# Performance work log

Measured on AMD Instinct MI355X. Metric: run time of the kernel, lower is better.

The kernel has to match this reference:

```python
import jax, jax.numpy as jnp
import numpy as np

N = 100000      # nodes
E = 3200000     # edges (avg degree 32)
DU = 256        # unary_channels
DP = 256        # pairwise_channels (== out_channels, required by fusion cat)
H = 64          # hidden_channels = out_channels // 4
DO = 256        # out_channels
STEPS = 1
EPS = 1e-5      # BatchNorm eps (torch default)


def _bn(h, gamma, beta):
    # BatchNorm1d, training-mode batch stats (biased variance, as torch normalizes)
    mu = jnp.mean(h, axis=0)
    var = jnp.var(h, axis=0)
    return gamma * (h - mu) * jax.lax.rsqrt(var + EPS) + beta


def setup_inputs() -> dict:
    key = jax.random.key(0)
    ks = jax.random.split(key, 12)
    edge_index = jax.random.randint(ks[0], (2, E), 0, N, dtype=jnp.int64)
    return {
        "x": jax.random.normal(ks[1], (N, DU), dtype=jnp.float32),
        "y": jax.random.normal(ks[2], (N, DP), dtype=jnp.float32),
        "pos": jax.random.normal(ks[3], (N, 3), dtype=jnp.float32),
        "edge_index": edge_index,
        "Wu": jax.random.normal(ks[4], (DU, H), dtype=jnp.float32) / np.sqrt(DU),
        "gu": jnp.ones((H,), jnp.float32), "bu": jnp.zeros((H,), jnp.float32),
        "Wp": jax.random.normal(ks[5], (DP, H), dtype=jnp.float32) / np.sqrt(DP),
        "gp": jnp.ones((H,), jnp.float32), "bp": jnp.zeros((H,), jnp.float32),
        "c": jnp.eye(H, dtype=jnp.float32) + 0.1 * jax.random.normal(ks[6], (H, H), dtype=jnp.float32),
        "Wm": jax.random.normal(ks[7], (H, DO), dtype=jnp.float32) / np.sqrt(H),
        "gm": jnp.ones((DO,), jnp.float32), "bm": jnp.zeros((DO,), jnp.float32),
        "Wf": jax.random.normal(ks[8], (2 * DO, DO), dtype=jnp.float32) / np.sqrt(2 * DO),
        "gf": jnp.ones((DO,), jnp.float32), "bf": jnp.zeros((DO,), jnp.float32),
    }


def reference(x, y, pos, edge_index, Wu, gu, bu, Wp, gp, bp, c, Wm, gm, bm, Wf, gf, bf):
    i, j = edge_index[0], edge_index[1]
    # unary / pairwise embeddings (Linear no-bias + BN)
    xu = _bn(x @ Wu, gu, bu)                      # [N, H]
    su = _bn(y @ Wp, gp, bp)                      # [N, H]
    # edge logits: -||s_i - s_j||^2, softmax grouped by destination i
    d = su[i] - su[j]                             # [E, H]
    logit = -jnp.sum(d * d, axis=1, keepdims=True)  # [E, 1]
    m = jax.ops.segment_max(logit, i, num_segments=N)
    ex = jnp.exp(logit - m[i])
    denom = jax.ops.segment_sum(ex, i, num_segments=N)
    s = ex / (denom[i] + 1e-16)                   # [E, 1] edge softmax weights
    # CRF mean-field iterations with linear solve
    z = xu
    C = c.T @ c                                   # [H, H]
    Minv = jnp.linalg.inv(jnp.eye(H, dtype=x.dtype) + C)
    h = xu
    for _ in range(STEPS):
        agg = jax.ops.segment_sum(s * h[j], i, num_segments=N)  # gather-scale-scatter
        h = (z + agg @ C) @ Minv
    # output heads
    h = jax.nn.leaky_relu(_bn(h @ Wm, gm, bm))
    out = jax.nn.leaky_relu(_bn(jnp.concatenate([h, y], axis=-1) @ Wf, gf, bf))
    return out
```

## Files before the change

kernel.cpp:

```cpp
#include <hip/hip_runtime.h>
#include <hip/hip_fp16.h>
#include <math.h>

typedef unsigned short u16;
typedef short s16x8 __attribute__((ext_vector_type(8)));
typedef unsigned short u16x8 __attribute__((ext_vector_type(8)));
typedef _Float16 f16x8 __attribute__((ext_vector_type(8)));
typedef float f32x4 __attribute__((ext_vector_type(4)));

__device__ __forceinline__ float bf2f(u16 u) {
  unsigned x = ((unsigned)u) << 16;
  return __uint_as_float(x);
}
__device__ __forceinline__ u16 f2bf(float f) {
  unsigned x = __float_as_uint(f);
  unsigned r = x + 0x7FFFu + ((x >> 16) & 1u);
  return (u16)(r >> 16);
}
__device__ __forceinline__ u16 f2h(float f) {
  __half h = __float2half_rn(f);
  return *reinterpret_cast<u16*>(&h);
}

static const size_t OFF_MINV   = 0;
static const size_t OFF_AU     = 32ull * 1024;
static const size_t OFF_BUE    = 32ull * 1024 + 256;
static const size_t OFF_AP     = 32ull * 1024 + 512;
static const size_t OFF_APBE   = 32ull * 1024 + 768;
static const size_t OFF_AM     = 36ull * 1024;
static const size_t OFF_BM     = 37ull * 1024;
static const size_t OFF_AF     = 38ull * 1024;
static const size_t OFF_BF     = 39ull * 1024;
static const size_t OFF_BTOT   = 40ull * 1024;
static const size_t OFF_BOFF   = 44ull * 1024;
static const size_t OFF_WUT    = 64ull * 1024;
static const size_t OFF_WMT    = 128ull * 1024;
static const size_t OFF_WFT    = 192ull * 1024;
static const size_t OFF_WPH    = 512ull * 1024;
static const size_t OFF_PART1A = 1ull  * 1024 * 1024;
static const size_t OFF_PART1B = 1ull  * 1024 * 1024 + 512 * 1024;
static const size_t OFF_PART2A = 2ull  * 1024 * 1024;
static const size_t OFF_PART2B = 2ull  * 1024 * 1024 + 512 * 1024;
static const size_t OFF_ROWPTR = 3ull  * 1024 * 1024;
static const size_t OFF_BLKCNT = 5ull  * 1024 * 1024;
static const size_t OFF_SRCJ   = 18ull * 1024 * 1024;
static const size_t OFF_U      = 44ull * 1024 * 1024;
static const size_t OFF_P      = 70ull * 1024 * 1024;
static const size_t OFF_PS     = 109ull * 1024 * 1024;
static const size_t OFF_H2     = 122ull * 1024 * 1024;

#define NBLK_BIN 1024

__global__ __launch_bounds__(256) void k_prep(const float* __restrict__ c,
                                              float* __restrict__ minv_out) {
  __shared__ float CC[4096];
  __shared__ float aug[64 * 129];
  __shared__ float fs[64];
  float* cl = aug;
  int t = threadIdx.x;
  for (int idx = t; idx < 4096; idx += 256) cl[idx] = c[idx];
  __syncthreads();
  for (int idx = t; idx < 4096; idx += 256) {
    int a = idx >> 6, b = idx & 63;
    float s = (a == b) ? 1.f : 0.f;
    for (int k = 0; k < 64; ++k) s += cl[k * 64 + a] * cl[k * 64 + b];
    CC[idx] = s;
  }
  __syncthreads();
  for (int idx = t; idx < 8192; idx += 256) {
    int r = idx >> 7, cc = idx & 127;
    aug[r * 129 + cc] = (cc < 64) ? CC[r * 64 + cc] : (((cc - 64) == r) ? 1.f : 0.f);
  }
  __syncthreads();
  int cloc = t & 127;
  int rbase = t >> 7;
  for (int p = 0; p < 64; ++p) {
    if (t < 64) fs[t] = (t == p) ? 0.f : aug[t * 129 + p] / aug[p * 129 + p];
    __syncthreads();
    float pc = aug[p * 129 + cloc];
#pragma unroll
    for (int rr = 0; rr < 64; rr += 2) {
      int r = rr + rbase;
      aug[r * 129 + cloc] -= fs[r] * pc;
    }
    __syncthreads();
  }
  for (int idx = t; idx < 4096; idx += 256) {
    int r = idx >> 6, cc = idx & 63;
    minv_out[idx] = aug[r * 129 + 64 + cc] / aug[r * 129 + r];
  }
}

__global__ __launch_bounds__(256) void k_tcvt_all(const float* __restrict__ Wu, const float* __restrict__ Wm,
                                                  const float* __restrict__ Wf, const float* __restrict__ Wp,
                                                  u16* __restrict__ WUT, u16* __restrict__ WMT,
                                                  u16* __restrict__ WFT, u16* __restrict__ WPH) {
  int b = blockIdx.x, t = threadIdx.x;
  if (b < 64) {
    int i = b * 256 + t;
    int k = i >> 6, n = i & 63;
    WUT[(size_t)n * 256 + k] = f2bf(Wu[i]);
  } else if (b < 128) {
    int i = (b - 64) * 256 + t;
    int k = i >> 8, n = i & 255;
    WMT[(size_t)n * 64 + k] = f2bf(Wm[i]);
  } else if (b < 640) {
    int i = (b - 128) * 256 + t;
    int k = i >> 8, n = i & 255;
    WFT[(size_t)n * 512 + k] = f2bf(Wf[i]);
  } else {
    int i = (b - 640) * 256 + t;
    int k = i >> 6, n = i & 63;
    WPH[(size_t)n * 256 + k] = f2h(Wp[i]);
  }
}

__global__ __launch_bounds__(256) void kA1(const int* __restrict__ ei, int E, int chunk,
                                           int* __restrict__ blockCnt, int nbk) {
  __shared__ int c[512];
  int t = threadIdx.x, bid = blockIdx.x;
  c[t] = 0; c[t + 256] = 0;
  __syncthreads();
  int e0 = bid * chunk, e1 = min(E, e0 + chunk);
  for (int e = e0 + t; e < e1; e += 256) atomicAdd(&c[ei[e] >> 8], 1);
  __syncthreads();
  for (int b = t; b < nbk; b += 256) blockCnt[(size_t)bid * nbk + b] = c[b];
}

__global__ __launch_bounds__(256) void kA2(int* __restrict__ blockCnt, int nbk,
                                           int* __restrict__ bucketTot) {
  int b = blockIdx.x, t = threadIdx.x;
  int base = t * 4;
  int v0 = blockCnt[(size_t)(base + 0) * nbk + b];
  int v1 = blockCnt[(size_t)(base + 1) * nbk + b];
  int v2 = blockCnt[(size_t)(base + 2) * nbk + b];
  int v3 = blockCnt[(size_t)(base + 3) * nbk + b];
  int s1 = v0 + v1, s2 = s1 + v2, tot = s2 + v3;
  __shared__ int ps[256];
  ps[t] = tot;
  __syncthreads();
  for (int off = 1; off < 256; off <<= 1) {
    int a = (t >= off) ? ps[t - off] : 0;
    __syncthreads();
    ps[t] += a;
    __syncthreads();
  }
  int ex = (t > 0) ? ps[t - 1] : 0;
  blockCnt[(size_t)(base + 0) * nbk + b] = ex;
  blockCnt[(size_t)(base + 1) * nbk + b] = ex + v0;
  blockCnt[(size_t)(base + 2) * nbk + b] = ex + s1;
  blockCnt[(size_t)(base + 3) * nbk + b] = ex + s2;
  if (t == 255) bucketTot[b] = ps[255];
}

__global__ __launch_bounds__(512) void kA2b(const int* __restrict__ bucketTot,
                                            int* __restrict__ bucketOff, int nbk) {
  __shared__ int s[512];
  int t = threadIdx.x;
  s[t] = (t < nbk) ? bucketTot[t] : 0;
  __syncthreads();
  for (int off = 1; off < 512; off <<= 1) {
    int a = (t >= off) ? s[t - off] : 0;
    __syncthreads();
    s[t] += a;
    __syncthreads();
  }
  if (t == 0) bucketOff[0] = 0;
  if (t < nbk) bucketOff[t + 1] = s[t];
}

__global__ __launch_bounds__(256) void kA3(const int* __restrict__ ei, const int* __restrict__ ej,
                                           int E, int chunk,
                                           const int* __restrict__ blockExc,
                                           const int* __restrict__ bucketOff,
                                           int nbk, unsigned* __restrict__ tmp) {
  __shared__ int c[512], off[512], gb[512], cur[512];
  __shared__ uint2 stage[4096];
  int t = threadIdx.x, bid = blockIdx.x;
  c[t] = 0; c[t + 256] = 0;
  __syncthreads();
  int e0 = bid * chunk, e1 = min(E, e0 + chunk);
  int m = e1 - e0;
  for (int e = e0 + t; e < e1; e += 256) atomicAdd(&c[ei[e] >> 8], 1);
  __syncthreads();
  int v0 = c[t], v1 = c[t + 256];
  off[t] = v0; off[t + 256] = v1;
  __syncthreads();
  for (int o = 1; o < 512; o <<= 1) {
    int a0 = (t >= o) ? off[t - o] : 0;
    int a1 = ((t + 256) >= o) ? off[t + 256 - o] : 0;
    __syncthreads();
    off[t] += a0; off[t + 256] += a1;
    __syncthreads();
  }
  int ex0 = off[t] - v0, ex1 = off[t + 256] - v1;
  if (t < nbk)
    gb[t] = bucketOff[t] + blockExc[(size_t)bid * nbk + t] - ex0;
  if (t + 256 < nbk)
    gb[t + 256] = bucketOff[t + 256] + blockExc[(size_t)bid * nbk + t + 256] - ex1;
  cur[t] = ex0; cur[t + 256] = ex1;
  __syncthreads();
  for (int e = e0 + t; e < e1; e += 256) {
    int i = ei[e];
    int p = atomicAdd(&cur[i >> 8], 1);
    stage[p] = make_uint2((unsigned)i, (unsigned)ej[e]);
  }
  __syncthreads();
  for (int s = t; s < m; s += 256) {
    uint2 v = stage[s];
    tmp[gb[v.x >> 8] + s] = ((v.x & 255u) << 24) | v.y;
  }
}

#define BCAP 12288
__global__ __launch_bounds__(256) void kB(const unsigned* __restrict__ tmp,
                                          const int* __restrict__ bucketOff,
                                          int nbk, int N, int E,
                                          int* __restrict__ rowptr, int* __restrict__ srcj) {
  __shared__ int cnt[256], sc[256], cur[256];
  __shared__ int jbuf[BCAP];
  int b = blockIdx.x, t = threadIdx.x;
  int nb0 = b << 8;
  int e0 = bucketOff[b], e1 = bucketOff[b + 1];
  int m = e1 - e0;
  cnt[t] = 0;
  __syncthreads();
  for (int s = t; s < m; s += 256) atomicAdd(&cnt[tmp[e0 + s] >> 24], 1);
  __syncthreads();
  int v = cnt[t];
  sc[t] = v;
  __syncthreads();
  for (int off = 1; off < 256; off <<= 1) {
    int a = (t >= off) ? sc[t - off] : 0;
    __syncthreads();
// ... 110 lines not shown
          if constexpr (FP16) {
            f16x8 af = *(const f16x8*)pa;
            f16x8 bf = *(const f16x8*)pb;
            acc[m][n] = __builtin_amdgcn_mfma_f32_16x16x32_f16(af, bf, acc[m][n], 0, 0, 0);
          } else {
            s16x8 af = *(const s16x8*)pa;
            s16x8 bf = *(const s16x8*)pb;
            acc[m][n] = __builtin_amdgcn_mfma_f32_16x16x32_bf16(af, bf, acc[m][n], 0, 0, 0);
          }
        }
      }
    }
  };

  loadTile(0);
  dswrite(0);
  __syncthreads();
  for (int kk = 0; kk < nK; ++kk) {
    int b = kk & 1;
    if (kk + 1 < nK) loadTile(kk + 1);
    compute(b);
    if (kk + 1 < nK) { dswrite(b ^ 1); __syncthreads(); }
  }

#pragma unroll
  for (int m = 0; m < 4; ++m) {
#pragma unroll
    for (int n = 0; n < FN; ++n) {
      int col = n0 + wc * WN + n * 16 + lr;
#pragma unroll
      for (int q = 0; q < 4; ++q) {
        int row = m0 + wr * 64 + m * 16 + lk * 4 + q;
        if (row < M) {
          if constexpr (OBF) Cb[(size_t)row * ldC + col] = f2bf(acc[m][n][q]);
          else               Cf[(size_t)row * ldC + col] = acc[m][n][q];
        }
      }
    }
  }

  if constexpr (STATS) {
    __syncthreads();
    float* sb = (float*)&lds[0][0];
#pragma unroll
    for (int n = 0; n < FN; ++n) {
      float s1 = 0.f, s2 = 0.f;
#pragma unroll
      for (int m = 0; m < 4; ++m)
#pragma unroll
        for (int q = 0; q < 4; ++q) {
          int row = m0 + wr * 64 + m * 16 + lk * 4 + q;
          float v = (row < M) ? acc[m][n][q] : 0.f;
          s1 += v; s2 += v * v;
        }
      s1 += __shfl_xor(s1, 16); s2 += __shfl_xor(s2, 16);
      s1 += __shfl_xor(s1, 32); s2 += __shfl_xor(s2, 32);
      if (lk == 0) {
        int c = wc * WN + n * 16 + lr;
        sb[(wr * BN + c) * 2 + 0] = s1;
        sb[(wr * BN + c) * 2 + 1] = s2;
      }
    }
    __syncthreads();
    if (t < BN) {
      float s1 = sb[t * 2]     + sb[(BN + t) * 2];
      float s2 = sb[t * 2 + 1] + sb[(BN + t) * 2 + 1];
      p1[(size_t)blockIdx.x * ncTot + n0 + t] = s1;
      p2[(size_t)blockIdx.x * ncTot + n0 + t] = s2;
// ... 200 lines not shown
    }
  }
}

__global__ __launch_bounds__(256) void k_reduce_fin(const float* __restrict__ part1,
                                                    const float* __restrict__ part2,
                                                    int nb, int C, float invN,
                                                    const float* __restrict__ gamma,
                                                    const float* __restrict__ beta,
                                                    float* __restrict__ a_out,
                                                    float* __restrict__ b_out) {
  int c = blockIdx.x;
  int t = threadIdx.x;
  float s1 = 0.f, s2 = 0.f;
  for (int b = t; b < nb; b += 256) {
    s1 += part1[(size_t)b * C + c];
    s2 += part2[(size_t)b * C + c];
  }
  for (int m = 32; m; m >>= 1) { s1 += __shfl_xor(s1, m); s2 += __shfl_xor(s2, m); }
  __shared__ float l1[4], l2[4];
  if ((t & 63) == 0) { l1[t >> 6] = s1; l2[t >> 6] = s2; }
  __syncthreads();
  if (t == 0) {
    s1 = l1[0] + l1[1] + l1[2] + l1[3];
    s2 = l2[0] + l2[1] + l2[2] + l2[3];
    float mu  = s1 * invN;
    float var = s2 * invN - mu * mu;
    float a = gamma[c] * rsqrtf(var + 1e-5f);
    a_out[c] = a;
    b_out[c] = beta[c] - mu * a;
  }
}

__global__ __launch_bounds__(256) void k_scaleP(const float* __restrict__ P, const float* __restrict__ ap,
                                                __half* __restrict__ PS, int n8) {
  for (int i = blockIdx.x * 256 + threadIdx.x; i < n8; i += gridDim.x * 256) {
    int c0 = (i & 7) * 8;
    float4 s0 = *(const float4*)(ap + c0), s1 = *(const float4*)(ap + c0 + 4);
    float4 a = ((const float4*)P)[i * 2];
    float4 b = ((const float4*)P)[i * 2 + 1];
    __half2 o0 = __floats2half2_rn(a.x * s0.x, a.y * s0.y);
    __half2 o1 = __floats2half2_rn(a.z * s0.z, a.w * s0.w);
    __half2 o2 = __floats2half2_rn(b.x * s1.x, b.y * s1.y);
    __half2 o3 = __floats2half2_rn(b.z * s1.z, b.w * s1.w);
    uint4 out;
    out.x = *(unsigned*)&o0; out.y = *(unsigned*)&o1;
    out.z = *(unsigned*)&o2; out.w = *(unsigned*)&o3;
    ((uint4*)PS)[i] = out;
  }
}

__global__ __launch_bounds__(256) void k_nodeall(const __half* __restrict__ PS,
                                                 const int* __restrict__ srcj,
                                                 const int* __restrict__ rowptr,
                                                 const u16* __restrict__ UB,
                                                 const float* __restrict__ au,
                                                 const float* __restrict__ bue,
                                                 const float* __restrict__ minv,
                                                 int N, u16* __restrict__ HB) {
  __shared__ float mS[4096];
  __shared__ float zma[4][64];
  int t = threadIdx.x;
  for (int idx = t; idx < 1024; idx += 256)
    ((float4*)mS)[idx] = ((const float4*)minv)[idx];
  __syncthreads();

  int lane = t & 63, wid = t >> 6;
  int node = blockIdx.x * 4 + wid;
  if (node >= N) return;

  int lane8 = lane & 7, g8 = lane >> 3;
  const uint4* P4 = (const uint4*)PS;
  uint4 uv = P4[(size_t)node * 8 + lane8];
  float2 u0 = __half22float2(*(const __half2*)&uv.x);
  float2 u1 = __half22float2(((const __half2*)&uv.x)[1]);
  float2 u2 = __half22float2(*(const __half2*)&uv.z);
  float2 u3 = __half22float2(((const __half2*)&uv.z)[1]);
  float psl = __half2float(PS[(size_t)node * 64 + lane]);
  int b0 = rowptr[node], b1 = rowptr[node + 1];
  int deg = b1 - b0;
  float aggv = 0.f;
  if (deg > 0) {
    int cnt = deg < 64 ? deg : 64;
    int jj = (lane < cnt) ? srcj[b0 + lane] : 0;
    float lg = -INFINITY;
    int capbase = lane & ~7;
    int capsrc  = (lane & 7) << 3;
    for (int ss = 0; ss < cnt; ss += 8) {
      int sl = ss + g8; if (sl >= cnt) sl = cnt - 1;
      int j = __shfl(jj, sl);
      uint4 vv = P4[(size_t)j * 8 + lane8];
      float2 v0 = __half22float2(*(const __half2*)&vv.x);
      float2 v1 = __half22float2(((const __half2*)&vv.x)[1]);
      float2 v2 = __half22float2(*(const __half2*)&vv.z);
      float2 v3 = __half22float2(((const __half2*)&vv.z)[1]);
      float d0 = u0.x - v0.x, d1 = u0.y - v0.y;
      float d2 = u1.x - v1.x, d3 = u1.y - v1.y;
      float d4 = u2.x - v2.x, d5 = u2.y - v2.y;
      float d6 = u3.x - v3.x, d7 = u3.y - v3.y;
      float p = d0*d0 + d1*d1 + d2*d2 + d3*d3 + d4*d4 + d5*d5 + d6*d6 + d7*d7;
      p += __shfl_xor(p, 1, 8);
      p += __shfl_xor(p, 2, 8);
      p += __shfl_xor(p, 4, 8);
      float val = __shfl(p, capsrc);
      if (ss == capbase && lane < cnt) lg = -val;
    }
    float mx = lg;
    for (int s = b0 + 64; s < b1; ++s) {
      int j = srcj[s];
      float d = psl - __half2float(PS[(size_t)j * 64 + lane]);
      float p = d * d;
      for (int m = 32; m; m >>= 1) p += __shfl_xor(p, m);
      mx = fmaxf(mx, -p);
    }
    for (int m = 32; m; m >>= 1) mx = fmaxf(mx, __shfl_xor(mx, m));
    float ex = (lane < cnt) ? __expf(lg - mx) : 0.f;
    float sm = ex;
    for (int s = b0 + 64; s < b1; ++s) {
      int j = srcj[s];
      float d = psl - __half2float(PS[(size_t)j * 64 + lane]);
      float p = d * d;
      for (int m = 32; m; m >>= 1) p += __shfl_xor(p, m);
      if (lane == 0) sm += __expf(-p - mx);
    }
    for (int m = 32; m; m >>= 1) sm += __shfl_xor(sm, m);
    float inv = 1.0f / (sm + 1e-16f);
    float w = ex * inv;
    float acc = 0.f;
    int ss = 0;
    for (; ss + 8 <= cnt; ss += 8) {
      int   j0 = __shfl(jj, ss),     j1 = __shfl(jj, ss + 1);
      int   j2 = __shfl(jj, ss + 2), j3 = __shfl(jj, ss + 3);
      int   j4 = __shfl(jj, ss + 4), j5 = __shfl(jj, ss + 5);
      int   j6 = __shfl(jj, ss + 6), j7 = __shfl(jj, ss + 7);
      float w0 = __shfl(w, ss),      w1 = __shfl(w, ss + 1);
      float w2 = __shfl(w, ss + 2),  w3 = __shfl(w, ss + 3);
      float w4 = __shfl(w, ss + 4),  w5 = __shfl(w, ss + 5);
      float w6 = __shfl(w, ss + 6),  w7 = __shfl(w, ss + 7);
      float v0 = bf2f(UB[(size_t)j0 * 64 + lane]);
      float v1 = bf2f(UB[(size_t)j1 * 64 + lane]);
      float v2 = bf2f(UB[(size_t)j2 * 64 + lane]);
      float v3 = bf2f(UB[(size_t)j3 * 64 + lane]);
      float v4 = bf2f(UB[(size_t)j4 * 64 + lane]);
      float v5 = bf2f(UB[(size_t)j5 * 64 + lane]);
      float v6 = bf2f(UB[(size_t)j6 * 64 + lane]);
      float v7 = bf2f(UB[(size_t)j7 * 64 + lane]);
      acc += w0 * v0 + w1 * v1 + w2 * v2 + w3 * v3;
      acc += w4 * v4 + w5 * v5 + w6 * v6 + w7 * v7;
    }
    for (; ss < cnt; ++ss) {
      int j0 = __shfl(jj, ss);
      float w0 = __shfl(w, ss);
      acc += w0 * bf2f(UB[(size_t)j0 * 64 + lane]);
    }
    for (int s = b0 + 64; s < b1; ++s) {
      int j = srcj[s];
      float d = psl - __half2float(PS[(size_t)j * 64 + lane]);
      float p = d * d;
      for (int m = 32; m; m >>= 1) p += __shfl_xor(p, m);
      acc += __expf(-p - mx) * inv * bf2f(UB[(size_t)j * 64 + lane]);
    }
    aggv = au[lane] * acc + bue[lane];
  }
  float z = au[lane] * bf2f(UB[(size_t)node * 64 + lane]) + bue[lane];
  zma[wid][lane] = z - aggv;
  float h = aggv;
#pragma unroll 8
  for (int k = 0; k < 64; ++k) h += zma[wid][k] * mS[k * 64 + lane];
  HB[(size_t)node * 64 + lane] = f2bf(h);
}

__global__ __launch_bounds__(256) void k_bnact16(const u16* __restrict__ raw, const float* __restrict__ af,
                                                 const float* __restrict__ bfp, float* __restrict__ out, int n8) {
  int i = blockIdx.x * 256 + threadIdx.x;
  int stride = gridDim.x * 256;
  for (; i < n8; i += stride) {
    int c0 = (i & 31) * 8;
    float av[8], bv[8];
    *(float4*)(av) = *(const float4*)(af + c0);  *(float4*)(av + 4) = *(const float4*)(af + c0 + 4);
    *(float4*)(bv) = *(const float4*)(bfp + c0); *(float4*)(bv + 4) = *(const float4*)(bfp + c0 + 4);
    u16x8 r = ((const u16x8*)raw)[i];
    float o[8];
#pragma unroll
    for (int j = 0; j < 8; ++j) {
      float v = bf2f((u16)r[j]) * av[j] + bv[j];
      o[j] = (v > 0.f) ? v : 0.01f * v;
    }
    ((float4*)out)[i * 2]     = *(float4*)(o);
    ((float4*)out)[i * 2 + 1] = *(float4*)(o + 4);
  }
// ... 16 lines not shown
  const float* gm   = (const float*)d_in[12];
  const float* bm   = (const float*)d_in[13];
  const float* Wf   = (const float*)d_in[14];
  const float* gf   = (const float*)d_in[15];
  const float* bfv  = (const float*)d_in[16];

  const int N = in_sizes[0] / 256;
  const int E = in_sizes[3] / 2;
  const int* ei = eidx;
  const int* ej = eidx + E;

  char* ws = (char*)d_ws;
  float* MINV  = (float*)(ws + OFF_MINV);
  float* AU    = (float*)(ws + OFF_AU);
  float* BUE   = (float*)(ws + OFF_BUE);
  float* AP    = (float*)(ws + OFF_AP);
  float* APBE  = (float*)(ws + OFF_APBE);
  float* AM    = (float*)(ws + OFF_AM);
  float* BM    = (float*)(ws + OFF_BM);
  float* AF    = (float*)(ws + OFF_AF);
  float* BF    = (float*)(ws + OFF_BF);
  int*   BTOT  = (int*)(ws + OFF_BTOT);
  int*   BOFF  = (int*)(ws + OFF_BOFF);
  u16*   WUT   = (u16*)(ws + OFF_WUT);
  u16*   WMT   = (u16*)(ws + OFF_WMT);
  u16*   WFT   = (u16*)(ws + OFF_WFT);
  u16*   WPH   = (u16*)(ws + OFF_WPH);
  float* PART1A= (float*)(ws + OFF_PART1A);
  float* PART1B= (float*)(ws + OFF_PART1B);
  float* PART2A= (float*)(ws + OFF_PART2A);
  float* PART2B= (float*)(ws + OFF_PART2B);
  int*   ROWPTR= (int*)(ws + OFF_ROWPTR);
  int*   BLKCNT= (int*)(ws + OFF_BLKCNT);
  u16*   HB    = (u16*)(ws + OFF_BLKCNT);
  int*   SRCJ  = (int*)(ws + OFF_SRCJ);
  u16*   RAWO  = (u16*)(ws + OFF_SRCJ);
  u16*   UBRAW = (u16*)(ws + OFF_U);
  unsigned* TMP= (unsigned*)(ws + OFF_P);
  float* P     = (float*)(ws + OFF_P);
  __half* PS   = (__half*)(ws + OFF_PS);
  u16*   H2    = (u16*)(ws + OFF_H2);

  const float invN = 1.0f / (float)N;
  const int mtiles   = (N + 127) / 128;
  const int n8_64    = N * 64 / 8;
  const int n8_256   = N * 256 / 8;
  const int nbk      = (N + 255) >> 8;
  const int chunk    = (E + NBLK_BIN - 1) / NBLK_BIN;

  k_prep<<<1, 256, 0, stream>>>(cIn, MINV);
  k_tcvt_all<<<704, 256, 0, stream>>>(Wu, Wm, Wf, Wp, WUT, WMT, WFT, WPH);

  kA1<<<NBLK_BIN, 256, 0, stream>>>(ei, E, chunk, BLKCNT, nbk);
  kA2<<<nbk, 256, 0, stream>>>(BLKCNT, nbk, BTOT);
  kA2b<<<1, 512, 0, stream>>>(BTOT, BOFF, nbk);
  kA3<<<NBLK_BIN, 256, 0, stream>>>(ei, ej, E, chunk, BLKCNT, BOFF, nbk, TMP);
  kB<<<nbk, 256, 0, stream>>>(TMP, BOFF, nbk, N, E, ROWPTR, SRCJ);

  k_mfma<64, 2, 1, 1, 0><<<dim3(mtiles, 1), 256, 0, stream>>>(
      nullptr, x, 256, 256, N, WUT, nullptr, UBRAW, 64, 64, PART1A, PART2A);

  k_mfma<64, 2, 0, 1, 1><<<dim3(mtiles, 1), 256, 0, stream>>>(
      nullptr, y, 256, 256, N, WPH, P, nullptr, 64, 64, PART1B, PART2B);

  k_reduce2<<<128, 256, 0, stream>>>(PART1A, PART2A, PART1B, PART2B, mtiles, invN,
                                     gu, bu, gp, bp, AU, BUE, AP, APBE);
  k_scaleP<<<1024, 256, 0, stream>>>(P, AP, PS, n8_64);

  k_nodeall<<<(N + 3) / 4, 256, 0, stream>>>(PS, SRCJ, ROWPTR, UBRAW, AU, BUE, MINV, N, HB);

  k_mfma2<0><<<mtiles, 512, 0, stream>>>(
      HB, 64, 64, N, nullptr, nullptr, nullptr, nullptr, WMT, H2, PART1A, PART2A);
  k_reduce_fin<<<256, 256, 0, stream>>>(PART1A, PART2A, mtiles, 256, invN, gm, bm, AM, BM);

  k_mfma2<1><<<mtiles, 512, 0, stream>>>(
      nullptr, 0, 512, N, H2, y, AM, BM, WFT, RAWO, PART1A, PART2A);
  k_reduce_fin<<<256, 256, 0, stream>>>(PART1A, PART2A, mtiles, 256, invN, gf, bfv, AF, BF);
  k_bnact16<<<2048, 256, 0, stream>>>(RAWO, AF, BF, (float*)d_out, n8_256);
}
```

Before: 527.3 us.

## Fold BN scale into node kernel, fuse prep kernels, reuse bin counts, unroll gathers

The pairwise GEMM now writes fp16 output directly, and the BN scale is applied inside the node kernel, so the separate fp32 P buffer and k_scaleP pass are gone. The matrix-inverse prep is merged into the weight-conversion launch as an extra block. The binning pass reuses per-block counts from kA1 instead of recounting edges in kA3, storing offsets in a new buffer. The node kernel also processes 16 neighbours per iteration in both the logit and aggregation loops to expose more memory parallelism. Storing unscaled fp16 values may change rounding, and the larger unroll raises register pressure.

```diff
diff --git a/kernel.cpp b/kernel.cpp
--- a/kernel.cpp
+++ b/kernel.cpp
@@ -43,6 +43,7 @@
 static const size_t OFF_PART2B = 2ull  * 1024 * 1024 + 512 * 1024;
 static const size_t OFF_ROWPTR = 3ull  * 1024 * 1024;
 static const size_t OFF_BLKCNT = 5ull  * 1024 * 1024;
+static const size_t OFF_BLKOFF = 7ull  * 1024 * 1024;
 static const size_t OFF_SRCJ   = 18ull * 1024 * 1024;
 static const size_t OFF_U      = 44ull * 1024 * 1024;
 static const size_t OFF_P      = 70ull * 1024 * 1024;
@@ -51,67 +52,67 @@
 
 #define NBLK_BIN 1024
 
-__global__ __launch_bounds__(256) void k_prep(const float* __restrict__ c,
-                                              float* __restrict__ minv_out) {
-  __shared__ float CC[4096];
-  __shared__ float aug[64 * 129];
-  __shared__ float fs[64];
-  float* cl = aug;
-  int t = threadIdx.x;
-  for (int idx = t; idx < 4096; idx += 256) cl[idx] = c[idx];
-  __syncthreads();
-  for (int idx = t; idx < 4096; idx += 256) {
-    int a = idx >> 6, b = idx & 63;
-    float s = (a == b) ? 1.f : 0.f;
-    for (int k = 0; k < 64; ++k) s += cl[k * 64 + a] * cl[k * 64 + b];
-    CC[idx] = s;
-  }
-  __syncthreads();
-  for (int idx = t; idx < 8192; idx += 256) {
-    int r = idx >> 7, cc = idx & 127;
-    aug[r * 129 + cc] = (cc < 64) ? CC[r * 64 + cc] : (((cc - 64) == r) ? 1.f : 0.f);
-  }
-  __syncthreads();
-  int cloc = t & 127;
-  int rbase = t >> 7;
-  for (int p = 0; p < 64; ++p) {
-    if (t < 64) fs[t] = (t == p) ? 0.f : aug[t * 129 + p] / aug[p * 129 + p];
-    __syncthreads();
-    float pc = aug[p * 129 + cloc];
-#pragma unroll
-    for (int rr = 0; rr < 64; rr += 2) {
-      int r = rr + rbase;
-      aug[r * 129 + cloc] -= fs[r] * pc;
-    }
-    __syncthreads();
-  }
-  for (int idx = t; idx < 4096; idx += 256) {
-    int r = idx >> 6, cc = idx & 63;
-    minv_out[idx] = aug[r * 129 + 64 + cc] / aug[r * 129 + r];
-  }
-}
-
-__global__ __launch_bounds__(256) void k_tcvt_all(const float* __restrict__ Wu, const float* __restrict__ Wm,
-                                                  const float* __restrict__ Wf, const float* __restrict__ Wp,
-                                                  u16* __restrict__ WUT, u16* __restrict__ WMT,
-                                                  u16* __restrict__ WFT, u16* __restrict__ WPH) {
+__global__ __launch_bounds__(256) void k_tcvt_prep(const float* __restrict__ Wu, const float* __restrict__ Wm,
+                                                   const float* __restrict__ Wf, const float* __restrict__ Wp,
+                                                   u16* __restrict__ WUT, u16* __restrict__ WMT,
+                                                   u16* __restrict__ WFT, u16* __restrict__ WPH,
+                                                   const float* __restrict__ c, float* __restrict__ minv_out) {
   int b = blockIdx.x, t = threadIdx.x;
   if (b < 64) {
     int i = b * 256 + t;
     int k = i >> 6, n = i & 63;
     WUT[(size_t)n * 256 + k] = f2bf(Wu[i]);
+    return;
   } else if (b < 128) {
     int i = (b - 64) * 256 + t;
     int k = i >> 8, n = i & 255;
     WMT[(size_t)n * 64 + k] = f2bf(Wm[i]);
+    return;
   } else if (b < 640) {
     int i = (b - 128) * 256 + t;
     int k = i >> 8, n = i & 255;
     WFT[(size_t)n * 512 + k] = f2bf(Wf[i]);
-  } else {
+    return;
+  } else if (b < 704) {
     int i = (b - 640) * 256 + t;
     int k = i >> 6, n = i & 63;
     WPH[(size_t)n * 256 + k] = f2h(Wp[i]);
+    return;
+  }
+  __shared__ float CC[4096];
+  __shared__ float aug[64 * 129];
+  __shared__ float fs[64];
+  float* cl = aug;
+  for (int idx = t; idx < 4096; idx += 256) cl[idx] = c[idx];
+  __syncthreads();
+  for (int idx = t; idx < 4096; idx += 256) {
+    int a = idx >> 6, bb = idx & 63;
+    float s = (a == bb) ? 1.f : 0.f;
+    for (int k = 0; k < 64; ++k) s += cl[k * 64 + a] * cl[k * 64 + bb];
+    CC[idx] = s;
+  }
+  __syncthreads();
+  for (int idx = t; idx < 8192; idx += 256) {
+    int r = idx >> 7, cc = idx & 127;
+    aug[r * 129 + cc] = (cc < 64) ? CC[r * 64 + cc] : (((cc - 64) == r) ? 1.f : 0.f);
+  }
+  __syncthreads();
+  int cloc = t & 127;
+  int rbase = t >> 7;
+  for (int p = 0; p < 64; ++p) {
+    if (t < 64) fs[t] = (t == p) ? 0.f : aug[t * 129 + p] / aug[p * 129 + p];
+    __syncthreads();
+    float pc = aug[p * 129 + cloc];
+#pragma unroll
+    for (int rr = 0; rr < 64; rr += 2) {
+      int r = rr + rbase;
+      aug[r * 129 + cloc] -= fs[r] * pc;
+    }
+    __syncthreads();
+  }
+  for (int idx = t; idx < 4096; idx += 256) {
+    int r = idx >> 6, cc = idx & 63;
+    minv_out[idx] = aug[r * 129 + 64 + cc] / aug[r * 129 + r];
   }
 }
 
@@ -127,8 +128,8 @@
   for (int b = t; b < nbk; b += 256) blockCnt[(size_t)bid * nbk + b] = c[b];
 }
 
-__global__ __launch_bounds__(256) void kA2(int* __restrict__ blockCnt, int nbk,
-                                           int* __restrict__ bucketTot) {
+__global__ __launch_bounds__(256) void kA2(const int* __restrict__ blockCnt, int nbk,
+                                           int* __restrict__ blkOff, int* __restrict__ bucketTot) {
   int b = blockIdx.x, t = threadIdx.x;
   int base = t * 4;
   int v0 = blockCnt[(size_t)(base + 0) * nbk + b];
@@ -146,10 +147,10 @@
     __syncthreads();
   }
   int ex = (t > 0) ? ps[t - 1] : 0;
-  blockCnt[(size_t)(base + 0) * nbk + b] = ex;
-  blockCnt[(size_t)(base + 1) * nbk + b] = ex + v0;
-  blockCnt[(size_t)(base + 2) * nbk + b] = ex + s1;
-  blockCnt[(size_t)(base + 3) * nbk + b] = ex + s2;
+  blkOff[(size_t)(base + 0) * nbk + b] = ex;
+  blkOff[(size_t)(base + 1) * nbk + b] = ex + v0;
+  blkOff[(size_t)(base + 2) * nbk + b] = ex + s1;
+  blkOff[(size_t)(base + 3) * nbk + b] = ex + s2;
   if (t == 255) bucketTot[b] = ps[255];
 }
 
@@ -171,19 +172,15 @@
 
 __global__ __launch_bounds__(256) void kA3(const int* __restrict__ ei, const int* __restrict__ ej,
                                            int E, int chunk,
-                                           const int* __restrict__ blockExc,
+                                           const int* __restrict__ blockCnt,
+                                           const int* __restrict__ blkOff,
                                            const int* __restrict__ bucketOff,
                                            int nbk, unsigned* __restrict__ tmp) {
-  __shared__ int c[512], off[512], gb[512], cur[512];
+  __shared__ int off[512], gb[512], cur[512];
   __shared__ uint2 stage[4096];
   int t = threadIdx.x, bid = blockIdx.x;
-  c[t] = 0; c[t + 256] = 0;
-  __syncthreads();
-  int e0 = bid * chunk, e1 = min(E, e0 + chunk);
-  int m = e1 - e0;
-  for (int e = e0 + t; e < e1; e += 256) atomicAdd(&c[ei[e] >> 8], 1);
-  __syncthreads();
-  int v0 = c[t], v1 = c[t + 256];
+  int v0 = (t < nbk) ? blockCnt[(size_t)bid * nbk + t] : 0;
+  int v1 = (t + 256 < nbk) ? blockCnt[(size_t)bid * nbk + t + 256] : 0;
   off[t] = v0; off[t + 256] = v1;
   __syncthreads();
   for (int o = 1; o < 512; o <<= 1) {
@@ -195,11 +192,13 @@
   }
   int ex0 = off[t] - v0, ex1 = off[t + 256] - v1;
   if (t < nbk)
-    gb[t] = bucketOff[t] + blockExc[(size_t)bid * nbk + t] - ex0;
+    gb[t] = bucketOff[t] + blkOff[(size_t)bid * nbk + t] - ex0;
   if (t + 256 < nbk)
-    gb[t + 256] = bucketOff[t + 256] + blockExc[(size_t)bid * nbk + t + 256] - ex1;
+    gb[t + 256] = bucketOff[t + 256] + blkOff[(size_t)bid * nbk + t + 256] - ex1;
   cur[t] = ex0; cur[t + 256] = ex1;
   __syncthreads();
+  int e0 = bid * chunk, e1 = min(E, e0 + chunk);
+  int m = e1 - e0;
   for (int e = e0 + t; e < e1; e += 256) {
     int i = ei[e];
     int p = atomicAdd(&cur[i >> 8], 1);
@@ -376,8 +375,9 @@
       for (int q = 0; q < 4; ++q) {
         int row = m0 + wr * 64 + m * 16 + lk * 4 + q;
         if (row < M) {
-          if constexpr (OBF) Cb[(size_t)row * ldC + col] = f2bf(acc[m][n][q]);
-          else               Cf[(size_t)row * ldC + col] = acc[m][n][q];
+          if constexpr (OBF == 2)      Cb[(size_t)row * ldC + col] = f2h(acc[m][n][q]);
+          else if constexpr (OBF == 1) Cb[(size_t)row * ldC + col] = f2bf(acc[m][n][q]);
+          else                         Cf[(size_t)row * ldC + col] = acc[m][n][q];
         }
       }
     }
@@ -644,30 +644,13 @@
   }
 }
 
-__global__ __launch_bounds__(256) void k_scaleP(const float* __restrict__ P, const float* __restrict__ ap,
-                                                __half* __restrict__ PS, int n8) {
-  for (int i = blockIdx.x * 256 + threadIdx.x; i < n8; i += gridDim.x * 256) {
-    int c0 = (i & 7) * 8;
-    float4 s0 = *(const float4*)(ap + c0), s1 = *(const float4*)(ap + c0 + 4);
-    float4 a = ((const float4*)P)[i * 2];
-    float4 b = ((const float4*)P)[i * 2 + 1];
-    __half2 o0 = __floats2half2_rn(a.x * s0.x, a.y * s0.y);
-    __half2 o1 = __floats2half2_rn(a.z * s0.z, a.w * s0.w);
-    __half2 o2 = __floats2half2_rn(b.x * s1.x, b.y * s1.y);
-    __half2 o3 = __floats2half2_rn(b.z * s1.z, b.w * s1.w);
-    uint4 out;
-    out.x = *(unsigned*)&o0; out.y = *(unsigned*)&o1;
-    out.z = *(unsigned*)&o2; out.w = *(unsigned*)&o3;
-    ((uint4*)PS)[i] = out;
-  }
-}
-
 __global__ __launch_bounds__(256) void k_nodeall(const __half* __restrict__ PS,
                                                  const int* __restrict__ srcj,
                                                  const int* __restrict__ rowptr,
                                                  const u16* __restrict__ UB,
                                                  const float* __restrict__ au,
                                                  const float* __restrict__ bue,
+                                                 const float* __restrict__ ap,
                                                  const float* __restrict__ minv,
                                                  int N, u16* __restrict__ HB) {
   __shared__ float mS[4096];
@@ -683,11 +666,17 @@
 
   int lane8 = lane & 7, g8 = lane >> 3;
   const uint4* P4 = (const uint4*)PS;
+  float av[8];
+  *(float4*)(av)     = *(const float4*)(ap + lane8 * 8);
+  *(float4*)(av + 4) = *(const float4*)(ap + lane8 * 8 + 4);
+  float apl = ap[lane];
   uint4 uv = P4[(size_t)node * 8 + lane8];
   float2 u0 = __half22float2(*(const __half2*)&uv.x);
   float2 u1 = __half22float2(((const __half2*)&uv.x)[1]);
   float2 u2 = __half22float2(*(const __half2*)&uv.z);
   float2 u3 = __half22float2(((const __half2*)&uv.z)[1]);
+  u0.x *= av[0]; u0.y *= av[1]; u1.x *= av[2]; u1.y *= av[3];
+  u2.x *= av[4]; u2.y *= av[5]; u3.x *= av[6]; u3.y *= av[7];
   float psl = __half2float(PS[(size_t)node * 64 + lane]);
   int b0 = rowptr[node], b1 = rowptr[node + 1];
   int deg = b1 - b0;
@@ -698,29 +687,53 @@
     float lg = -INFINITY;
     int capbase = lane & ~7;
     int capsrc  = (lane & 7) << 3;
-    for (int ss = 0; ss < cnt; ss += 8) {
-      int sl = ss + g8; if (sl >= cnt) sl = cnt - 1;
-      int j = __shfl(jj, sl);
-      uint4 vv = P4[(size_t)j * 8 + lane8];
+
+    auto logit8 = [&](uint4 vv) -> float {
       float2 v0 = __half22float2(*(const __half2*)&vv.x);
       float2 v1 = __half22float2(((const __half2*)&vv.x)[1]);
       float2 v2 = __half22float2(*(const __half2*)&vv.z);
       float2 v3 = __half22float2(((const __half2*)&vv.z)[1]);
-      float d0 = u0.x - v0.x, d1 = u0.y - v0.y;
-      float d2 = u1.x - v1.x, d3 = u1.y - v1.y;
-      float d4 = u2.x - v2.x, d5 = u2.y - v2.y;
-      float d6 = u3.x - v3.x, d7 = u3.y - v3.y;
-      float p = d0*d0 + d1*d1 + d2*d2 + d3*d3 + d4*d4 + d5*d5 + d6*d6 + d7*d7;
-      p += __shfl_xor(p, 1, 8);
-      p += __shfl_xor(p, 2, 8);
-      p += __shfl_xor(p, 4, 8);
-      float val = __shfl(p, capsrc);
-      if (ss == capbase && lane < cnt) lg = -val;
+      float d0 = fmaf(-av[0], v0.x, u0.x), d1 = fmaf(-av[1], v0.y, u0.y);
+      float d2 = fmaf(-av[2], v1.x, u1.x), d3 = fmaf(-av[3], v1.y, u1.y);
+      float d4 = fmaf(-av[4], v2.x, u2.x), d5 = fmaf(-av[5], v2.y, u2.y);
+      float d6 = fmaf(-av[6], v3.x, u3.x), d7 = fmaf(-av[7], v3.y, u3.y);
+      return d0*d0 + d1*d1 + d2*d2 + d3*d3 + d4*d4 + d5*d5 + d6*d6 + d7*d7;
+    };
+
+    int ss = 0;
+    while (ss < cnt) {
+      if (ss + 16 <= cnt) {
+        int jA = __shfl(jj, ss + g8);
+        int jB = __shfl(jj, ss + 8 + g8);
+        uint4 vvA = P4[(size_t)jA * 8 + lane8];
+        uint4 vvB = P4[(size_t)jB * 8 + lane8];
+        float pA = logit8(vvA);
+        float pB = logit8(vvB);
+        pA += __shfl_xor(pA, 1, 8); pB += __shfl_xor(pB, 1, 8);
+        pA += __shfl_xor(pA, 2, 8); pB += __shfl_xor(pB, 2, 8);
+        pA += __shfl_xor(pA, 4, 8); pB += __shfl_xor(pB, 4, 8);
+        float valA = __shfl(pA, capsrc);
+        float valB = __shfl(pB, capsrc);
+        if (ss == capbase && lane < cnt) lg = -valA;
+        if (ss + 8 == capbase && lane < cnt) lg = -valB;
+        ss += 16;
+      } else {
+        int sl = ss + g8; if (sl >= cnt) sl = cnt - 1;
+        int j = __shfl(jj, sl);
+        uint4 vv = P4[(size_t)j * 8 + lane8];
+        float p = logit8(vv);
+        p += __shfl_xor(p, 1, 8);
+        p += __shfl_xor(p, 2, 8);
+        p += __shfl_xor(p, 4, 8);
+        float val = __shfl(p, capsrc);
+        if (ss == capbase && lane < cnt) lg = -val;
+        ss += 8;
+      }
     }
     float mx = lg;
     for (int s = b0 + 64; s < b1; ++s) {
       int j = srcj[s];
-      float d = psl - __half2float(PS[(size_t)j * 64 + lane]);
+      float d = apl * (psl - __half2float(PS[(size_t)j * 64 + lane]));
       float p = d * d;
       for (int m = 32; m; m >>= 1) p += __shfl_xor(p, m);
       mx = fmaxf(mx, -p);
@@ -730,7 +743,7 @@
     float sm = ex;
     for (int s = b0 + 64; s < b1; ++s) {
       int j = srcj[s];
-      float d = psl - __half2float(PS[(size_t)j * 64 + lane]);
+      float d = apl * (psl - __half2float(PS[(size_t)j * 64 + lane]));
       float p = d * d;
       for (int m = 32; m; m >>= 1) p += __shfl_xor(p, m);
       if (lane == 0) sm += __expf(-p - mx);
@@ -739,26 +752,26 @@
     float inv = 1.0f / (sm + 1e-16f);
     float w = ex * inv;
     float acc = 0.f;
-    int ss = 0;
+    ss = 0;
+    for (; ss + 16 <= cnt; ss += 16) {
+      int jv[16]; float wv[16];
+#pragma unroll
+      for (int q = 0; q < 16; ++q) { jv[q] = __shfl(jj, ss + q); wv[q] = __shfl(w, ss + q); }
+      float vv[16];
+#pragma unroll
+      for (int q = 0; q < 16; ++q) vv[q] = bf2f(UB[(size_t)jv[q] * 64 + lane]);
+#pragma unroll
+      for (int q = 0; q < 16; ++q) acc += wv[q] * vv[q];
+    }
     for (; ss + 8 <= cnt; ss += 8) {
-      int   j0 = __shfl(jj, ss),     j1 = __shfl(jj, ss + 1);
-      int   j2 = __shfl(jj, ss + 2), j3 = __shfl(jj, ss + 3);
-      int   j4 = __shfl(jj, ss + 4), j5 = __shfl(jj, ss + 5);
-      int   j6 = __shfl(jj, ss + 6), j7 = __shfl(jj, ss + 7);
-      float w0 = __shfl(w, ss),      w1 = __shfl(w, ss + 1);
-      float w2 = __shfl(w, ss + 2),  w3 = __shfl(w, ss + 3);
-      float w4 = __shfl(w, ss + 4),  w5 = __shfl(w, ss + 5);
-      float w6 = __shfl(w, ss + 6),  w7 = __shfl(w, ss + 7);
-      float v0 = bf2f(UB[(size_t)j0 * 64 + lane]);
-      float v1 = bf2f(UB[(size_t)j1 * 64 + lane]);
-      float v2 = bf2f(UB[(size_t)j2 * 64 + lane]);
-      float v3 = bf2f(UB[(size_t)j3 * 64 + lane]);
-      float v4 = bf2f(UB[(size_t)j4 * 64 + lane]);
-      float v5 = bf2f(UB[(size_t)j5 * 64 + lane]);
-      float v6 = bf2f(UB[(size_t)j6 * 64 + lane]);
-      float v7 = bf2f(UB[(size_t)j7 * 64 + lane]);
-      acc += w0 * v0 + w1 * v1 + w2 * v2 + w3 * v3;
-      acc += w4 * v4 + w5 * v5 + w6 * v6 + w7 * v7;
+      int jv[8]; float wv[8];
+#pragma unroll
+      for (int q = 0; q < 8; ++q) { jv[q] = __shfl(jj, ss + q); wv[q] = __shfl(w, ss + q); }
+      float vv[8];
+#pragma unroll
+      for (int q = 0; q < 8; ++q) vv[q] = bf2f(UB[(size_t)jv[q] * 64 + lane]);
+#pragma unroll
+      for (int q = 0; q < 8; ++q) acc += wv[q] * vv[q];
     }
     for (; ss < cnt; ++ss) {
       int j0 = __shfl(jj, ss);
@@ -767,7 +780,7 @@
     }
     for (int s = b0 + 64; s < b1; ++s) {
       int j = srcj[s];
-      float d = psl - __half2float(PS[(size_t)j * 64 + lane]);
+      float d = apl * (psl - __half2float(PS[(size_t)j * 64 + lane]));
       float p = d * d;
       for (int m = 32; m; m >>= 1) p += __shfl_xor(p, m);
       acc += __expf(-p - mx) * inv * bf2f(UB[(size_t)j * 64 + lane]);
@@ -850,42 +863,39 @@
   float* PART2B= (float*)(ws + OFF_PART2B);
   int*   ROWPTR= (int*)(ws + OFF_ROWPTR);
   int*   BLKCNT= (int*)(ws + OFF_BLKCNT);
+  int*   BLKOFF= (int*)(ws + OFF_BLKOFF);
   u16*   HB    = (u16*)(ws + OFF_BLKCNT);
   int*   SRCJ  = (int*)(ws + OFF_SRCJ);
   u16*   RAWO  = (u16*)(ws + OFF_SRCJ);
   u16*   UBRAW = (u16*)(ws + OFF_U);
   unsigned* TMP= (unsigned*)(ws + OFF_P);
-  float* P     = (float*)(ws + OFF_P);
   __half* PS   = (__half*)(ws + OFF_PS);
   u16*   H2    = (u16*)(ws + OFF_H2);
 
   const float invN = 1.0f / (float)N;
   const int mtiles   = (N + 127) / 128;
-  const int n8_64    = N * 64 / 8;
   const int n8_256   = N * 256 / 8;
   const int nbk      = (N + 255) >> 8;
   const int chunk    = (E + NBLK_BIN - 1) / NBLK_BIN;
 
-  k_prep<<<1, 256, 0, stream>>>(cIn, MINV);
-  k_tcvt_all<<<704, 256, 0, stream>>>(Wu, Wm, Wf, Wp, WUT, WMT, WFT, WPH);
+  k_tcvt_prep<<<705, 256, 0, stream>>>(Wu, Wm, Wf, Wp, WUT, WMT, WFT, WPH, cIn, MINV);
 
   kA1<<<NBLK_BIN, 256, 0, stream>>>(ei, E, chunk, BLKCNT, nbk);
-  kA2<<<nbk, 256, 0, stream>>>(BLKCNT, nbk, BTOT);
+  kA2<<<nbk, 256, 0, stream>>>(BLKCNT, nbk, BLKOFF, BTOT);
   kA2b<<<1, 512, 0, stream>>>(BTOT, BOFF, nbk);
-  kA3<<<NBLK_BIN, 256, 0, stream>>>(ei, ej, E, chunk, BLKCNT, BOFF, nbk, TMP);
+  kA3<<<NBLK_BIN, 256, 0, stream>>>(ei, ej, E, chunk, BLKCNT, BLKOFF, BOFF, nbk, TMP);
   kB<<<nbk, 256, 0, stream>>>(TMP, BOFF, nbk, N, E, ROWPTR, SRCJ);
 
   k_mfma<64, 2, 1, 1, 0><<<dim3(mtiles, 1), 256, 0, stream>>>(
       nullptr, x, 256, 256, N, WUT, nullptr, UBRAW, 64, 64, PART1A, PART2A);
 
-  k_mfma<64, 2, 0, 1, 1><<<dim3(mtiles, 1), 256, 0, stream>>>(
-      nullptr, y, 256, 256, N, WPH, P, nullptr, 64, 64, PART1B, PART2B);
+  k_mfma<64, 2, 2, 1, 1><<<dim3(mtiles, 1), 256, 0, stream>>>(
+      nullptr, y, 256, 256, N, WPH, nullptr, (u16*)PS, 64, 64, PART1B, PART2B);
 
   k_reduce2<<<128, 256, 0, stream>>>(PART1A, PART2A, PART1B, PART2B, mtiles, invN,
                                      gu, bu, gp, bp, AU, BUE, AP, APBE);
-  k_scaleP<<<1024, 256, 0, stream>>>(P, AP, PS, n8_64);
-
-  k_nodeall<<<(N + 3) / 4, 256, 0, stream>>>(PS, SRCJ, ROWPTR, UBRAW, AU, BUE, MINV, N, HB);
+
+  k_nodeall<<<(N + 3) / 4, 256, 0, stream>>>(PS, SRCJ, ROWPTR, UBRAW, AU, BUE, AP, MINV, N, HB);
 
   k_mfma2<0><<<mtiles, 512, 0, stream>>>(
       HB, 64, 64, N, nullptr, nullptr, nullptr, nullptr, WMT, H2, PART1A, PART2A);
```

New measurement: 549.9 us. +4.3%, slower.

## Merge prep kernels, reuse bin counts in scatter, store pairwise GEMM as fp16

Applied to the files above, without the earlier changes.

The matrix-inverse prep is folded into the weight-conversion kernel as an extra block, which removes one launch. The binning scatter kernel now reads the per-block counts saved by the counting pass instead of recounting edges with shared atomics, so kA2 writes its offsets to a separate buffer. The pairwise GEMM now writes fp16 straight into PS, and the scale kernel rescales in place. That halves its traffic and drops the fp32 P buffer, with a small precision risk from rounding before the scale is applied.

```diff
diff --git a/kernel.cpp b/kernel.cpp
--- a/kernel.cpp
+++ b/kernel.cpp
@@ -43,6 +43,7 @@
 static const size_t OFF_PART2B = 2ull  * 1024 * 1024 + 512 * 1024;
 static const size_t OFF_ROWPTR = 3ull  * 1024 * 1024;
 static const size_t OFF_BLKCNT = 5ull  * 1024 * 1024;
+static const size_t OFF_BLKOFF = 7ull  * 1024 * 1024;
 static const size_t OFF_SRCJ   = 18ull * 1024 * 1024;
 static const size_t OFF_U      = 44ull * 1024 * 1024;
 static const size_t OFF_P      = 70ull * 1024 * 1024;
@@ -51,67 +52,67 @@
 
 #define NBLK_BIN 1024
 
-__global__ __launch_bounds__(256) void k_prep(const float* __restrict__ c,
-                                              float* __restrict__ minv_out) {
-  __shared__ float CC[4096];
-  __shared__ float aug[64 * 129];
-  __shared__ float fs[64];
-  float* cl = aug;
-  int t = threadIdx.x;
-  for (int idx = t; idx < 4096; idx += 256) cl[idx] = c[idx];
-  __syncthreads();
-  for (int idx = t; idx < 4096; idx += 256) {
-    int a = idx >> 6, b = idx & 63;
-    float s = (a == b) ? 1.f : 0.f;
-    for (int k = 0; k < 64; ++k) s += cl[k * 64 + a] * cl[k * 64 + b];
-    CC[idx] = s;
-  }
-  __syncthreads();
-  for (int idx = t; idx < 8192; idx += 256) {
-    int r = idx >> 7, cc = idx & 127;
-    aug[r * 129 + cc] = (cc < 64) ? CC[r * 64 + cc] : (((cc - 64) == r) ? 1.f : 0.f);
-  }
-  __syncthreads();
-  int cloc = t & 127;
-  int rbase = t >> 7;
-  for (int p = 0; p < 64; ++p) {
-    if (t < 64) fs[t] = (t == p) ? 0.f : aug[t * 129 + p] / aug[p * 129 + p];
-    __syncthreads();
-    float pc = aug[p * 129 + cloc];
-#pragma unroll
-    for (int rr = 0; rr < 64; rr += 2) {
-      int r = rr + rbase;
-      aug[r * 129 + cloc] -= fs[r] * pc;
-    }
-    __syncthreads();
-  }
-  for (int idx = t; idx < 4096; idx += 256) {
-    int r = idx >> 6, cc = idx & 63;
-    minv_out[idx] = aug[r * 129 + 64 + cc] / aug[r * 129 + r];
-  }
-}
-
-__global__ __launch_bounds__(256) void k_tcvt_all(const float* __restrict__ Wu, const float* __restrict__ Wm,
-                                                  const float* __restrict__ Wf, const float* __restrict__ Wp,
-                                                  u16* __restrict__ WUT, u16* __restrict__ WMT,
-                                                  u16* __restrict__ WFT, u16* __restrict__ WPH) {
+__global__ __launch_bounds__(256) void k_tcvt_prep(const float* __restrict__ Wu, const float* __restrict__ Wm,
+                                                   const float* __restrict__ Wf, const float* __restrict__ Wp,
+                                                   u16* __restrict__ WUT, u16* __restrict__ WMT,
+                                                   u16* __restrict__ WFT, u16* __restrict__ WPH,
+                                                   const float* __restrict__ c, float* __restrict__ minv_out) {
   int b = blockIdx.x, t = threadIdx.x;
   if (b < 64) {
     int i = b * 256 + t;
     int k = i >> 6, n = i & 63;
     WUT[(size_t)n * 256 + k] = f2bf(Wu[i]);
+    return;
   } else if (b < 128) {
     int i = (b - 64) * 256 + t;
     int k = i >> 8, n = i & 255;
     WMT[(size_t)n * 64 + k] = f2bf(Wm[i]);
+    return;
   } else if (b < 640) {
     int i = (b - 128) * 256 + t;
     int k = i >> 8, n = i & 255;
     WFT[(size_t)n * 512 + k] = f2bf(Wf[i]);
-  } else {
+    return;
+  } else if (b < 704) {
     int i = (b - 640) * 256 + t;
     int k = i >> 6, n = i & 63;
     WPH[(size_t)n * 256 + k] = f2h(Wp[i]);
+    return;
+  }
+  __shared__ float CC[4096];
+  __shared__ float aug[64 * 129];
+  __shared__ float fs[64];
+  float* cl = aug;
+  for (int idx = t; idx < 4096; idx += 256) cl[idx] = c[idx];
+  __syncthreads();
+  for (int idx = t; idx < 4096; idx += 256) {
+    int a = idx >> 6, bb = idx & 63;
+    float s = (a == bb) ? 1.f : 0.f;
+    for (int k = 0; k < 64; ++k) s += cl[k * 64 + a] * cl[k * 64 + bb];
+    CC[idx] = s;
+  }
+  __syncthreads();
+  for (int idx = t; idx < 8192; idx += 256) {
+    int r = idx >> 7, cc = idx & 127;
+    aug[r * 129 + cc] = (cc < 64) ? CC[r * 64 + cc] : (((cc - 64) == r) ? 1.f : 0.f);
+  }
+  __syncthreads();
+  int cloc = t & 127;
+  int rbase = t >> 7;
+  for (int p = 0; p < 64; ++p) {
+    if (t < 64) fs[t] = (t == p) ? 0.f : aug[t * 129 + p] / aug[p * 129 + p];
+    __syncthreads();
+    float pc = aug[p * 129 + cloc];
+#pragma unroll
+    for (int rr = 0; rr < 64; rr += 2) {
+      int r = rr + rbase;
+      aug[r * 129 + cloc] -= fs[r] * pc;
+    }
+    __syncthreads();
+  }
+  for (int idx = t; idx < 4096; idx += 256) {
+    int r = idx >> 6, cc = idx & 63;
+    minv_out[idx] = aug[r * 129 + 64 + cc] / aug[r * 129 + r];
   }
 }
 
@@ -127,8 +128,8 @@
   for (int b = t; b < nbk; b += 256) blockCnt[(size_t)bid * nbk + b] = c[b];
 }
 
-__global__ __launch_bounds__(256) void kA2(int* __restrict__ blockCnt, int nbk,
-                                           int* __restrict__ bucketTot) {
+__global__ __launch_bounds__(256) void kA2(const int* __restrict__ blockCnt, int nbk,
+                                           int* __restrict__ blkOff, int* __restrict__ bucketTot) {
   int b = blockIdx.x, t = threadIdx.x;
   int base = t * 4;
   int v0 = blockCnt[(size_t)(base + 0) * nbk + b];
@@ -146,10 +147,10 @@
     __syncthreads();
   }
   int ex = (t > 0) ? ps[t - 1] : 0;
-  blockCnt[(size_t)(base + 0) * nbk + b] = ex;
-  blockCnt[(size_t)(base + 1) * nbk + b] = ex + v0;
-  blockCnt[(size_t)(base + 2) * nbk + b] = ex + s1;
-  blockCnt[(size_t)(base + 3) * nbk + b] = ex + s2;
+  blkOff[(size_t)(base + 0) * nbk + b] = ex;
+  blkOff[(size_t)(base + 1) * nbk + b] = ex + v0;
+  blkOff[(size_t)(base + 2) * nbk + b] = ex + s1;
+  blkOff[(size_t)(base + 3) * nbk + b] = ex + s2;
   if (t == 255) bucketTot[b] = ps[255];
 }
 
@@ -171,19 +172,15 @@
 
 __global__ __launch_bounds__(256) void kA3(const int* __restrict__ ei, const int* __restrict__ ej,
                                            int E, int chunk,
-                                           const int* __restrict__ blockExc,
+                                           const int* __restrict__ blockCnt,
+                                           const int* __restrict__ blkOff,
                                            const int* __restrict__ bucketOff,
                                            int nbk, unsigned* __restrict__ tmp) {
-  __shared__ int c[512], off[512], gb[512], cur[512];
+  __shared__ int off[512], gb[512], cur[512];
   __shared__ uint2 stage[4096];
   int t = threadIdx.x, bid = blockIdx.x;
-  c[t] = 0; c[t + 256] = 0;
-  __syncthreads();
-  int e0 = bid * chunk, e1 = min(E, e0 + chunk);
-  int m = e1 - e0;
-  for (int e = e0 + t; e < e1; e += 256) atomicAdd(&c[ei[e] >> 8], 1);
-  __syncthreads();
-  int v0 = c[t], v1 = c[t + 256];
+  int v0 = (t < nbk) ? blockCnt[(size_t)bid * nbk + t] : 0;
+  int v1 = (t + 256 < nbk) ? blockCnt[(size_t)bid * nbk + t + 256] : 0;
   off[t] = v0; off[t + 256] = v1;
   __syncthreads();
   for (int o = 1; o < 512; o <<= 1) {
@@ -195,11 +192,13 @@
   }
   int ex0 = off[t] - v0, ex1 = off[t + 256] - v1;
   if (t < nbk)
-    gb[t] = bucketOff[t] + blockExc[(size_t)bid * nbk + t] - ex0;
+    gb[t] = bucketOff[t] + blkOff[(size_t)bid * nbk + t] - ex0;
   if (t + 256 < nbk)
-    gb[t + 256] = bucketOff[t + 256] + blockExc[(size_t)bid * nbk + t + 256] - ex1;
+    gb[t + 256] = bucketOff[t + 256] + blkOff[(size_t)bid * nbk + t + 256] - ex1;
   cur[t] = ex0; cur[t + 256] = ex1;
   __syncthreads();
+  int e0 = bid * chunk, e1 = min(E, e0 + chunk);
+  int m = e1 - e0;
   for (int e = e0 + t; e < e1; e += 256) {
     int i = ei[e];
     int p = atomicAdd(&cur[i >> 8], 1);
@@ -376,8 +375,9 @@
       for (int q = 0; q < 4; ++q) {
         int row = m0 + wr * 64 + m * 16 + lk * 4 + q;
         if (row < M) {
-          if constexpr (OBF) Cb[(size_t)row * ldC + col] = f2bf(acc[m][n][q]);
-          else               Cf[(size_t)row * ldC + col] = acc[m][n][q];
+          if constexpr (OBF == 2)      Cb[(size_t)row * ldC + col] = f2h(acc[m][n][q]);
+          else if constexpr (OBF == 1) Cb[(size_t)row * ldC + col] = f2bf(acc[m][n][q]);
+          else                         Cf[(size_t)row * ldC + col] = acc[m][n][q];
         }
       }
     }
@@ -644,20 +644,21 @@
   }
 }
 
-__global__ __launch_bounds__(256) void k_scaleP(const float* __restrict__ P, const float* __restrict__ ap,
-                                                __half* __restrict__ PS, int n8) {
+__global__ __launch_bounds__(256) void k_scaleP16(__half* __restrict__ PS, const float* __restrict__ ap, int n8) {
   for (int i = blockIdx.x * 256 + threadIdx.x; i < n8; i += gridDim.x * 256) {
     int c0 = (i & 7) * 8;
-    float4 s0 = *(const float4*)(ap + c0), s1 = *(const float4*)(ap + c0 + 4);
-    float4 a = ((const float4*)P)[i * 2];
-    float4 b = ((const float4*)P)[i * 2 + 1];
-    __half2 o0 = __floats2half2_rn(a.x * s0.x, a.y * s0.y);
-    __half2 o1 = __floats2half2_rn(a.z * s0.z, a.w * s0.w);
-    __half2 o2 = __floats2half2_rn(b.x * s1.x, b.y * s1.y);
-    __half2 o3 = __floats2half2_rn(b.z * s1.z, b.w * s1.w);
+    float av[8];
+    *(float4*)(av)     = *(const float4*)(ap + c0);
+    *(float4*)(av + 4) = *(const float4*)(ap + c0 + 4);
+    uint4 in = ((const uint4*)PS)[i];
+    __half2* hp = (__half2*)&in;
     uint4 out;
-    out.x = *(unsigned*)&o0; out.y = *(unsigned*)&o1;
-    out.z = *(unsigned*)&o2; out.w = *(unsigned*)&o3;
+    __half2* op = (__half2*)&out;
+#pragma unroll
+    for (int j = 0; j < 4; ++j) {
+      float2 f = __half22float2(hp[j]);
+      op[j] = __floats2half2_rn(f.x * av[j * 2], f.y * av[j * 2 + 1]);
+    }
     ((uint4*)PS)[i] = out;
   }
 }
@@ -850,12 +851,12 @@
   float* PART2B= (float*)(ws + OFF_PART2B);
   int*   ROWPTR= (int*)(ws + OFF_ROWPTR);
   int*   BLKCNT= (int*)(ws + OFF_BLKCNT);
+  int*   BLKOFF= (int*)(ws + OFF_BLKOFF);
   u16*   HB    = (u16*)(ws + OFF_BLKCNT);
   int*   SRCJ  = (int*)(ws + OFF_SRCJ);
   u16*   RAWO  = (u16*)(ws + OFF_SRCJ);
   u16*   UBRAW = (u16*)(ws + OFF_U);
   unsigned* TMP= (unsigned*)(ws + OFF_P);
-  float* P     = (float*)(ws + OFF_P);
   __half* PS   = (__half*)(ws + OFF_PS);
   u16*   H2    = (u16*)(ws + OFF_H2);
 
@@ -866,24 +867,23 @@
   const int nbk      = (N + 255) >> 8;
   const int chunk    = (E + NBLK_BIN - 1) / NBLK_BIN;
 
-  k_prep<<<1, 256, 0, stream>>>(cIn, MINV);
-  k_tcvt_all<<<704, 256, 0, stream>>>(Wu, Wm, Wf, Wp, WUT, WMT, WFT, WPH);
+  k_tcvt_prep<<<705, 256, 0, stream>>>(Wu, Wm, Wf, Wp, WUT, WMT, WFT, WPH, cIn, MINV);
 
   kA1<<<NBLK_BIN, 256, 0, stream>>>(ei, E, chunk, BLKCNT, nbk);
-  kA2<<<nbk, 256, 0, stream>>>(BLKCNT, nbk, BTOT);
+  kA2<<<nbk, 256, 0, stream>>>(BLKCNT, nbk, BLKOFF, BTOT);
   kA2b<<<1, 512, 0, stream>>>(BTOT, BOFF, nbk);
-  kA3<<<NBLK_BIN, 256, 0, stream>>>(ei, ej, E, chunk, BLKCNT, BOFF, nbk, TMP);
+  kA3<<<NBLK_BIN, 256, 0, stream>>>(ei, ej, E, chunk, BLKCNT, BLKOFF, BOFF, nbk, TMP);
   kB<<<nbk, 256, 0, stream>>>(TMP, BOFF, nbk, N, E, ROWPTR, SRCJ);
 
   k_mfma<64, 2, 1, 1, 0><<<dim3(mtiles, 1), 256, 0, stream>>>(
       nullptr, x, 256, 256, N, WUT, nullptr, UBRAW, 64, 64, PART1A, PART2A);
 
-  k_mfma<64, 2, 0, 1, 1><<<dim3(mtiles, 1), 256, 0, stream>>>(
-      nullptr, y, 256, 256, N, WPH, P, nullptr, 64, 64, PART1B, PART2B);
+  k_mfma<64, 2, 2, 1, 1><<<dim3(mtiles, 1), 256, 0, stream>>>(
+      nullptr, y, 256, 256, N, WPH, nullptr, (u16*)PS, 64, 64, PART1B, PART2B);
 
   k_reduce2<<<128, 256, 0, stream>>>(PART1A, PART2A, PART1B, PART2B, mtiles, invN,
                                      gu, bu, gp, bp, AU, BUE, AP, APBE);
-  k_scaleP<<<1024, 256, 0, stream>>>(P, AP, PS, n8_64);
+  k_scaleP16<<<1024, 256, 0, stream>>>(PS, AP, n8_64);
 
   k_nodeall<<<(N + 3) / 4, 256, 0, stream>>>(PS, SRCJ, ROWPTR, UBRAW, AU, BUE, MINV, N, HB);
 
```

Measured after the change: 514.5 us. -2.4%, faster.
